# Kernel tuning notes

Measured on AMD Instinct MI355X. Metric: run time of the kernel, lower is better.

## Reference

```python
import jax, jax.numpy as jnp
import numpy as np

MAX_ATOMS = 13   # forward hard-codes x[:, :13, :]
LEN = 100        # ll1 output width, conv kernel = 2*LEN


def setup_inputs() -> dict:
    key = jax.random.key(0)
    k0, k1, k2, k3, k4 = jax.random.split(key, 5)
    B, S, d_model = 8192, 13, 512
    x = jax.random.normal(k0, (B, S, d_model), dtype=jnp.float32)
    # ll1: Linear(d_model, 100)
    W1 = jax.random.normal(k1, (LEN, d_model), dtype=jnp.float32) / np.sqrt(d_model)
    b1 = jax.random.normal(k2, (LEN,), dtype=jnp.float32) * 0.01
    # conv: Conv2d(1, 4, kernel=(1,200), stride=(1,200)) == per-pair linear 200->4
    Wc = jax.random.normal(k3, (4, 2 * LEN), dtype=jnp.float32) / np.sqrt(2 * LEN)
    bc = jax.random.normal(k4, (4,), dtype=jnp.float32) * 0.01
    return {"x": x, "W1": W1, "b1": b1, "Wc": Wc, "bc": bc, "max_atoms": MAX_ATOMS}


def reference(x, W1, b1, Wc, bc, max_atoms):
    # ll1 on first MAX_ATOMS atom embeddings -> [B, A, 100]
    feat = x[:, :MAX_ATOMS] @ W1.T + b1
    # pairwise ordered concat: block (i,j) = [feat[min(i,j)], feat[max(i,j)]]
    i = jnp.arange(max_atoms)[:, None]
    j = jnp.arange(max_atoms)[None, :]
    lo = jnp.minimum(i, j)   # [A, A]
    hi = jnpomaximum = jnp.maximum(i, j)
    pair = jnp.concatenate([feat[:, lo], feat[:, hi]], axis=-1)  # [B, A, A, 200]
    # stride==kernel Conv2d == batched linear over each 200-wide block -> [B, A, A, 4]
    # (matches final_e.permute(0, 2, 3, 1) layout)
    return jnp.einsum("bijc,oc->bijo", pair, Wc) + bc
```

## Files before the change

kernel.cpp:

```cpp
#include <hip/hip_runtime.h>
#include <hip/hip_bf16.h>


#define NA 13
#define DM 512
#define NOH 8
#define LEN 100

typedef float fv4 __attribute__((ext_vector_type(4)));

__global__ __launch_bounds__(512) void precompute_M(
    const float* __restrict__ W1, const float* __restrict__ b1,
    const float* __restrict__ Wc, const float* __restrict__ bc,
    float* __restrict__ M, float* __restrict__ s) {
    __shared__ float W1s[LEN * 64];
    const int tid = threadIdx.x;
    const int d_base = blockIdx.x * 64;

#pragma unroll
    for (int r = 0; r < 4; ++r) {
        int idx = tid + r * 512;
        if (idx < LEN * 16) {
            int c = idx >> 4, d4 = idx & 15;
            *(fv4*)(W1s + c * 64 + d4 * 4) =
                *(const fv4*)(W1 + c * DM + d_base + d4 * 4);
        }
    }
    __syncthreads();

    const int oh = tid >> 6;
    const int d = tid & 63;
    const int o = oh & 3, half = oh >> 2;
    const float* wc = Wc + o * 200 + half * 100;

    float a0 = 0.f, a1 = 0.f, a2 = 0.f, a3 = 0.f;
#pragma unroll
    for (int c = 0; c < LEN; c += 4) {
        a0 = fmaf(wc[c + 0], W1s[(c + 0) * 64 + d], a0);
        a1 = fmaf(wc[c + 1], W1s[(c + 1) * 64 + d], a1);
        a2 = fmaf(wc[c + 2], W1s[(c + 2) * 64 + d], a2);
        a3 = fmaf(wc[c + 3], W1s[(c + 3) * 64 + d], a3);
    }
    M[oh * DM + d_base + d] = (a0 + a1) + (a2 + a3);

    if (blockIdx.x == 0) {
        float p = wc[d] * b1[d];
        if (d < LEN - 64) p = fmaf(wc[d + 64], b1[d + 64], p);
#pragma unroll
        for (int m = 32; m >= 1; m >>= 1) p += __shfl_xor(p, m, 64);
        if (d == 0) s[oh] = p + ((half == 0) ? bc[o] : 0.f);
    }
}

__global__ __launch_bounds__(256) void edge_main(
    const float* __restrict__ x, const float* __restrict__ M,
    const float* __restrict__ s, float* __restrict__ out) {
    const int b = blockIdx.x;
    const int lane = threadIdx.x & 63;
    const int wave = threadIdx.x >> 6;

    const float* xb = x + (size_t)b * (NA * DM);

    fv4 xA[4], xB[4];
#pragma unroll
    for (int k = 0; k < 4; ++k) {
        const int a = wave + 4 * k;
        if (a < NA) {
            xA[k] = *(const fv4*)(xb + a * DM + lane * 4);
            xB[k] = *(const fv4*)(xb + a * DM + 256 + lane * 4);
        }
    }

    fv4 mA[NOH], mB[NOH];
#pragma unroll
    for (int oh = 0; oh < NOH; ++oh) {
        mA[oh] = *(const fv4*)(M + oh * DM + lane * 4);
        mB[oh] = *(const fv4*)(M + oh * DM + 256 + lane * 4);
    }
    const float s_lane = s[lane & 7];

    const bool m1 = (lane & 1) != 0;
    const bool m2 = (lane & 2) != 0;
    const bool m4 = (lane & 4) != 0;

    __shared__ float G[NA][NOH];

#pragma unroll
    for (int k = 0; k < 4; ++k) {
        const int a = wave + 4 * k;
        if (a < NA) {
            float acc[NOH];
#pragma unroll
            for (int oh = 0; oh < NOH; ++oh) {
                float v = xA[k].x * mA[oh].x;
                v = fmaf(xA[k].y, mA[oh].y, v);
                v = fmaf(xA[k].z, mA[oh].z, v);
                v = fmaf(xA[k].w, mA[oh].w, v);
                v = fmaf(xB[k].x, mB[oh].x, v);
                v = fmaf(xB[k].y, mB[oh].y, v);
                v = fmaf(xB[k].z, mB[oh].z, v);
                v = fmaf(xB[k].w, mB[oh].w, v);
                acc[oh] = v;
            }
            float r1[4];
#pragma unroll
            for (int q = 0; q < 4; ++q) {
                float keep = m1 ? acc[2 * q + 1] : acc[2 * q];
                float send = m1 ? acc[2 * q]     : acc[2 * q + 1];
                r1[q] = keep + __shfl_xor(send, 1, 64);
            }
            float r2[2];
#pragma unroll
            for (int q = 0; q < 2; ++q) {
                float keep = m2 ? r1[2 * q + 1] : r1[2 * q];
                float send = m2 ? r1[2 * q]     : r1[2 * q + 1];
                r2[q] = keep + __shfl_xor(send, 2, 64);
            }
            float keep = m4 ? r2[1] : r2[0];
            float send = m4 ? r2[0] : r2[1];
            float t = keep + __shfl_xor(send, 4, 64);
            t += __shfl_xor(t, 8, 64);
            t += __shfl_xor(t, 16, 64);
            t += __shfl_xor(t, 32, 64);
            if (lane < NOH) G[a][lane] = t + s_lane;
        }
    }
    __syncthreads();

    const int t = threadIdx.x;
    if (t < NA * NA) {
        int i = t / NA, j = t % NA;
        int lo = i < j ? i : j;
        int hi = i < j ? j : i;
        fv4 v;
        v.x = G[lo][0] + G[hi][4];
        v.y = G[lo][1] + G[hi][5];
        v.z = G[lo][2] + G[hi][6];
        v.w = G[lo][3] + G[hi][7];
        ((fv4*)(out + (size_t)b * (NA * NA * 4)))[t] = v;
    }
}

extern "C" void kernel_launch(void* const* d_in, const int* in_sizes, int n_in,
                              void* d_out, int out_size, void* d_ws, size_t ws_size,
                              hipStream_t stream) {
    const float* x  = (const float*)d_in[0];
    const float* W1 = (const float*)d_in[1];
    const float* b1 = (const float*)d_in[2];
    const float* Wc = (const float*)d_in[3];
    const float* bc = (const float*)d_in[4];
    float* out = (float*)d_out;
    const int B = in_sizes[0] / (NA * DM);

    float* M = (float*)d_ws;
    float* s = M + NOH * DM;

    precompute_M<<<8, 512, 0, stream>>>(W1, b1, Wc, bc, M, s);
    edge_main<<<B, 256, 0, stream>>>(x, M, s, out);
}
```

Before: 46.39 us.

## Split edge kernel into per-wave batch dot kernel and separate combine kernel

Replaces the fused per-batch kernel with two kernels. The first assigns one wave per batch item, loops over all 13 atoms with double-buffered x loads, and writes the 13x8 projections to a workspace buffer. The second expands them into the 13x13x4 pair output. This removes the block-wide barrier and the idle waves in the original per-batch block, at the cost of an extra launch and a small global round trip for G. The old fused kernel is kept as a fallback when the workspace is too small.

```diff
diff --git a/kernel.cpp b/kernel.cpp
--- a/kernel.cpp
+++ b/kernel.cpp
@@ -52,6 +52,98 @@
     }
 }
 
+__global__ __launch_bounds__(256) void edge_dots(
+    const float* __restrict__ x, const float* __restrict__ M,
+    const float* __restrict__ s, float* __restrict__ G) {
+    const int lane = threadIdx.x & 63;
+    const int wave = threadIdx.x >> 6;
+    const int b = blockIdx.x * 4 + wave;
+
+    fv4 mA[NOH], mB[NOH];
+#pragma unroll
+    for (int oh = 0; oh < NOH; ++oh) {
+        mA[oh] = *(const fv4*)(M + oh * DM + lane * 4);
+        mB[oh] = *(const fv4*)(M + oh * DM + 256 + lane * 4);
+    }
+    const float s_lane = s[lane & 7];
+
+    const bool m1 = (lane & 1) != 0;
+    const bool m2 = (lane & 2) != 0;
+    const bool m4 = (lane & 4) != 0;
+
+    const float* xb = x + (size_t)b * (NA * DM);
+    float* gb = G + (size_t)b * (NA * NOH);
+
+    fv4 pA[2], pB[2];
+    pA[0] = *(const fv4*)(xb + lane * 4);
+    pB[0] = *(const fv4*)(xb + 256 + lane * 4);
+
+#pragma unroll
+    for (int a = 0; a < NA; ++a) {
+        const int cur = a & 1;
+        if (a < NA - 1) {
+            pA[cur ^ 1] = *(const fv4*)(xb + (a + 1) * DM + lane * 4);
+            pB[cur ^ 1] = *(const fv4*)(xb + (a + 1) * DM + 256 + lane * 4);
+        }
+        const fv4 xA = pA[cur];
+        const fv4 xB = pB[cur];
+        float acc[NOH];
+#pragma unroll
+        for (int oh = 0; oh < NOH; ++oh) {
+            float v = xA.x * mA[oh].x;
+            v = fmaf(xA.y, mA[oh].y, v);
+            v = fmaf(xA.z, mA[oh].z, v);
+            v = fmaf(xA.w, mA[oh].w, v);
+            v = fmaf(xB.x, mB[oh].x, v);
+            v = fmaf(xB.y, mB[oh].y, v);
+            v = fmaf(xB.z, mB[oh].z, v);
+            v = fmaf(xB.w, mB[oh].w, v);
+            acc[oh] = v;
+        }
+        float r1[4];
+#pragma unroll
+        for (int q = 0; q < 4; ++q) {
+            float keep = m1 ? acc[2 * q + 1] : acc[2 * q];
+            float send = m1 ? acc[2 * q]     : acc[2 * q + 1];
+            r1[q] = keep + __shfl_xor(send, 1, 64);
+        }
+        float r2[2];
+#pragma unroll
+        for (int q = 0; q < 2; ++q) {
+            float keep = m2 ? r1[2 * q + 1] : r1[2 * q];
+            float send = m2 ? r1[2 * q]     : r1[2 * q + 1];
+            r2[q] = keep + __shfl_xor(send, 2, 64);
+        }
+        float keep = m4 ? r2[1] : r2[0];
+        float send = m4 ? r2[0] : r2[1];
+        float t = keep + __shfl_xor(send, 4, 64);
+        t += __shfl_xor(t, 8, 64);
+        t += __shfl_xor(t, 16, 64);
+        t += __shfl_xor(t, 32, 64);
+        if (lane < NOH) gb[a * NOH + lane] = t + s_lane;
+    }
+}
+
+__global__ __launch_bounds__(256) void edge_combine(
+    const float* __restrict__ G, float* __restrict__ out) {
+    const int b = blockIdx.x;
+    const int t = threadIdx.x;
+    if (t < NA * NA) {
+        const float* gb = G + (size_t)b * (NA * NOH);
+        int i = t / NA, j = t % NA;
+        int lo = i < j ? i : j;
+        int hi = i < j ? j : i;
+        fv4 lov = *(const fv4*)(gb + lo * NOH);
+        fv4 hiv = *(const fv4*)(gb + hi * NOH + 4);
+        fv4 v;
+        v.x = lov.x + hiv.x;
+        v.y = lov.y + hiv.y;
+        v.z = lov.z + hiv.z;
+        v.w = lov.w + hiv.w;
+        ((fv4*)(out + (size_t)b * (NA * NA * 4)))[t] = v;
+    }
+}
+
 __global__ __launch_bounds__(256) void edge_main(
     const float* __restrict__ x, const float* __restrict__ M,
     const float* __restrict__ s, float* __restrict__ out) {
@@ -83,7 +175,7 @@
     const bool m2 = (lane & 2) != 0;
     const bool m4 = (lane & 4) != 0;
 
-    __shared__ float G[NA][NOH];
+    __shared__ float Gs[NA][NOH];
 
 #pragma unroll
     for (int k = 0; k < 4; ++k) {
@@ -122,7 +214,7 @@
             t += __shfl_xor(t, 8, 64);
             t += __shfl_xor(t, 16, 64);
             t += __shfl_xor(t, 32, 64);
-            if (lane < NOH) G[a][lane] = t + s_lane;
+            if (lane < NOH) Gs[a][lane] = t + s_lane;
         }
     }
     __syncthreads();
@@ -133,10 +225,10 @@
         int lo = i < j ? i : j;
         int hi = i < j ? j : i;
         fv4 v;
-        v.x = G[lo][0] + G[hi][4];
-        v.y = G[lo][1] + G[hi][5];
-        v.z = G[lo][2] + G[hi][6];
-        v.w = G[lo][3] + G[hi][7];
+        v.x = Gs[lo][0] + Gs[hi][4];
+        v.y = Gs[lo][1] + Gs[hi][5];
+        v.z = Gs[lo][2] + Gs[hi][6];
+        v.w = Gs[lo][3] + Gs[hi][7];
         ((fv4*)(out + (size_t)b * (NA * NA * 4)))[t] = v;
     }
 }
@@ -154,7 +246,15 @@
 
     float* M = (float*)d_ws;
     float* s = M + NOH * DM;
+    float* G = (float*)((char*)d_ws + 32768);
+
+    const size_t need = 32768 + (size_t)B * NA * NOH * sizeof(float);
 
     precompute_M<<<8, 512, 0, stream>>>(W1, b1, Wc, bc, M, s);
-    edge_main<<<B, 256, 0, stream>>>(x, M, s, out);
-}
+    if (ws_size >= need) {
+        edge_dots<<<B / 4, 256, 0, stream>>>(x, M, s, G);
+        edge_combine<<<B, 256, 0, stream>>>(G, out);
+    } else {
+        edge_main<<<B, 256, 0, stream>>>(x, M, s, out);
+    }
+}
```

Result: slower. 49.62 us (+7.0%).

## Assign one batch item per wave with double-buffered atom loads, drop block barrier

Applied to the files above, without the earlier changes.

Each wave now processes one whole batch element, looping over all 13 atoms with a two-deep register prefetch of the next atom's row. The output scatter is done per wave from a per-wave shared buffer, so the block-wide __syncthreads is removed and the grid shrinks by four. The goal is to cut barrier stalls and idle waves (previously 3 of 16 atom slots were empty) and to keep more loads in flight per wave. The cost is a longer serial dependency chain per wave, and B must be divisible by 4.

```diff
diff --git a/kernel.cpp b/kernel.cpp
--- a/kernel.cpp
+++ b/kernel.cpp
@@ -55,21 +55,17 @@
 __global__ __launch_bounds__(256) void edge_main(
     const float* __restrict__ x, const float* __restrict__ M,
     const float* __restrict__ s, float* __restrict__ out) {
-    const int b = blockIdx.x;
     const int lane = threadIdx.x & 63;
     const int wave = threadIdx.x >> 6;
+    const int b = blockIdx.x * 4 + wave;
 
     const float* xb = x + (size_t)b * (NA * DM);
 
-    fv4 xA[4], xB[4];
-#pragma unroll
-    for (int k = 0; k < 4; ++k) {
-        const int a = wave + 4 * k;
-        if (a < NA) {
-            xA[k] = *(const fv4*)(xb + a * DM + lane * 4);
-            xB[k] = *(const fv4*)(xb + a * DM + 256 + lane * 4);
-        }
-    }
+    fv4 pA0, pB0, pA1, pB1;
+    pA0 = *(const fv4*)(xb + lane * 4);
+    pB0 = *(const fv4*)(xb + 256 + lane * 4);
+    pA1 = *(const fv4*)(xb + DM + lane * 4);
+    pB1 = *(const fv4*)(xb + DM + 256 + lane * 4);
 
     fv4 mA[NOH], mB[NOH];
 #pragma unroll
@@ -83,61 +79,72 @@
     const bool m2 = (lane & 2) != 0;
     const bool m4 = (lane & 4) != 0;
 
-    __shared__ float G[NA][NOH];
+    __shared__ float GW[4][NA][NOH];
 
 #pragma unroll
-    for (int k = 0; k < 4; ++k) {
-        const int a = wave + 4 * k;
-        if (a < NA) {
-            float acc[NOH];
+    for (int a = 0; a < NA; ++a) {
+        const fv4 xA = (a & 1) ? pA1 : pA0;
+        const fv4 xB = (a & 1) ? pB1 : pB0;
+        if (a < NA - 2) {
+            if (a & 1) {
+                pA1 = *(const fv4*)(xb + (a + 2) * DM + lane * 4);
+                pB1 = *(const fv4*)(xb + (a + 2) * DM + 256 + lane * 4);
+            } else {
+                pA0 = *(const fv4*)(xb + (a + 2) * DM + lane * 4);
+                pB0 = *(const fv4*)(xb + (a + 2) * DM + 256 + lane * 4);
+            }
+        }
+        float acc[NOH];
 #pragma unroll
-            for (int oh = 0; oh < NOH; ++oh) {
-                float v = xA[k].x * mA[oh].x;
-                v = fmaf(xA[k].y, mA[oh].y, v);
-                v = fmaf(xA[k].z, mA[oh].z, v);
-                v = fmaf(xA[k].w, mA[oh].w, v);
-                v = fmaf(xB[k].x, mB[oh].x, v);
-                v = fmaf(xB[k].y, mB[oh].y, v);
-                v = fmaf(xB[k].z, mB[oh].z, v);
-                v = fmaf(xB[k].w, mB[oh].w, v);
-                acc[oh] = v;
-            }
-            float r1[4];
+        for (int oh = 0; oh < NOH; ++oh) {
+            float v = xA.x * mA[oh].x;
+            v = fmaf(xA.y, mA[oh].y, v);
+            v = fmaf(xA.z, mA[oh].z, v);
+            v = fmaf(xA.w, mA[oh].w, v);
+            v = fmaf(xB.x, mB[oh].x, v);
+            v = fmaf(xB.y, mB[oh].y, v);
+            v = fmaf(xB.z, mB[oh].z, v);
+            v = fmaf(xB.w, mB[oh].w, v);
+            acc[oh] = v;
+        }
+        float r1[4];
 #pragma unroll
-            for (int q = 0; q < 4; ++q) {
-                float keep = m1 ? acc[2 * q + 1] : acc[2 * q];
-                float send = m1 ? acc[2 * q]     : acc[2 * q + 1];
-                r1[q] = keep + __shfl_xor(send, 1, 64);
-            }
-            float r2[2];
+        for (int q = 0; q < 4; ++q) {
+            float keep = m1 ? acc[2 * q + 1] : acc[2 * q];
+            float send = m1 ? acc[2 * q]     : acc[2 * q + 1];
+            r1[q] = keep + __shfl_xor(send, 1, 64);
+        }
+        float r2[2];
 #pragma unroll
-            for (int q = 0; q < 2; ++q) {
-                float keep = m2 ? r1[2 * q + 1] : r1[2 * q];
-                float send = m2 ? r1[2 * q]     : r1[2 * q + 1];
-                r2[q] = keep + __shfl_xor(send, 2, 64);
-            }
-            float keep = m4 ? r2[1] : r2[0];
-            float send = m4 ? r2[0] : r2[1];
-            float t = keep + __shfl_xor(send, 4, 64);
-            t += __shfl_xor(t, 8, 64);
-            t += __shfl_xor(t, 16, 64);
-            t += __shfl_xor(t, 32, 64);
-            if (lane < NOH) G[a][lane] = t + s_lane;
+        for (int q = 0; q < 2; ++q) {
+            float keep = m2 ? r1[2 * q + 1] : r1[2 * q];
+            float send = m2 ? r1[2 * q]     : r1[2 * q + 1];
+            r2[q] = keep + __shfl_xor(send, 2, 64);
         }
+        float keep = m4 ? r2[1] : r2[0];
+        float send = m4 ? r2[0] : r2[1];
+        float t = keep + __shfl_xor(send, 4, 64);
+        t += __shfl_xor(t, 8, 64);
+        t += __shfl_xor(t, 16, 64);
+        t += __shfl_xor(t, 32, 64);
+        if (lane < NOH) GW[wave][a][lane] = t + s_lane;
     }
-    __syncthreads();
 
-    const int t = threadIdx.x;
-    if (t < NA * NA) {
-        int i = t / NA, j = t % NA;
-        int lo = i < j ? i : j;
-        int hi = i < j ? j : i;
-        fv4 v;
-        v.x = G[lo][0] + G[hi][4];
-        v.y = G[lo][1] + G[hi][5];
-        v.z = G[lo][2] + G[hi][6];
-        v.w = G[lo][3] + G[hi][7];
-        ((fv4*)(out + (size_t)b * (NA * NA * 4)))[t] = v;
+    fv4* outb = (fv4*)(out + (size_t)b * (NA * NA * 4));
+#pragma unroll
+    for (int r = 0; r < 3; ++r) {
+        const int t = lane + 64 * r;
+        if (t < NA * NA) {
+            int i = t / NA, j = t % NA;
+            int lo = i < j ? i : j;
+            int hi = i < j ? j : i;
+            fv4 v;
+            v.x = GW[wave][lo][0] + GW[wave][hi][4];
+            v.y = GW[wave][lo][1] + GW[wave][hi][5];
+            v.z = GW[wave][lo][2] + GW[wave][hi][6];
+            v.w = GW[wave][lo][3] + GW[wave][hi][7];
+            outb[t] = v;
+        }
     }
 }
 
@@ -156,5 +163,5 @@
     float* s = M + NOH * DM;
 
     precompute_M<<<8, 512, 0, stream>>>(W1, b1, Wc, bc, M, s);
-    edge_main<<<B, 256, 0, stream>>>(x, M, s, out);
+    edge_main<<<B / 4, 256, 0, stream>>>(x, M, s, out);
 }
```

Result: faster. 45.44 us, median of 2 (-2.0%).
